# Optimization experiments

Measured on AMD Instinct MI355X. Metric: run time of the kernel, lower is better.

## Reference

```python
import jax, jax.numpy as jnp
import numpy as np

B, S0, S1 = 4, 768, 256
T = S0 + S1
W0, W1 = 2048, 1024
N, K, H = 8, 1, 256  # num_heads, num_kv_heads (MQA), head_dim
G = N // K
MAX_WAVELENGTH = 10000.0
BIG_NEG = -2.3819763e+38


def _apply_rope(x, positions):
    """RoPE: positions [B,L] applied to x [B,L,heads,H]."""
    half = x.shape[-1] // 2
    freq_exponents = (2.0 / x.shape[-1]) * jnp.arange(half, dtype=jnp.float32)
    timescale = MAX_WAVELENGTH ** freq_exponents  # [half]
    radians = positions[..., None].astype(jnp.float32) / timescale  # [B,L,half]
    radians = radians[..., None, :]  # [B,L,1,half]
    sin, cos = jnp.sin(radians), jnp.cos(radians)
    x1, x2 = jnp.split(x.astype(jnp.float32), 2, axis=-1)
    res = jnp.concatenate([x1 * cos - x2 * sin, x2 * cos + x1 * sin], axis=-1)
    return res.astype(x.dtype)


def setup_inputs() -> dict:
    key = jax.random.key(0)
    ks = jax.random.split(key, 8)
    x0 = jax.random.normal(ks[0], (B, S0, W0), dtype=jnp.float32)
    x1 = jax.random.normal(ks[1], (B, S1, W1), dtype=jnp.float32)
    positions = jnp.broadcast_to(jnp.arange(T, dtype=jnp.int32)[None, :], (B, T))
    # causal mask [B,1,T,T]
    attn_mask = jnp.broadcast_to(jnp.tril(jnp.ones((T, T), dtype=bool))[None, None], (B, 1, T, T))
    # lecun_normal on the width (in) axis
    q0_w = jax.random.normal(ks[2], (N, W0, H), dtype=jnp.float32) / np.sqrt(W0)
    kv0_w = jax.random.normal(ks[3], (2, K, W0, H), dtype=jnp.float32) / np.sqrt(W0)
    out0_w = jax.random.normal(ks[4], (N, H, W0), dtype=jnp.float32) / np.sqrt(N * H)
    q1_w = jax.random.normal(ks[5], (N, W1, H), dtype=jnp.float32) / np.sqrt(W1)
    kv1_w = jax.random.normal(ks[6], (2, K, W1, H), dtype=jnp.float32) / np.sqrt(W1)
    out1_w = jax.random.normal(ks[7], (N, H, W1), dtype=jnp.float32) / np.sqrt(N * H)
    return {"x0": x0, "x1": x1, "positions": positions, "attn_mask": attn_mask,
            "q0_w": q0_w, "kv0_w": kv0_w, "out0_w": out0_w,
            "q1_w": q1_w, "kv1_w": kv1_w, "out1_w": out1_w}


def reference(x0, x1, positions, attn_mask, q0_w, kv0_w, out0_w, q1_w, kv1_w, out1_w):
    dtype = x0.dtype
    # per-modality QKV projections (num_kv_heads != num_heads branch)
    q0 = jnp.einsum('BTD,NDH->BTNH', x0, q0_w.astype(dtype))
    k0, v0 = jnp.einsum('BSD,2KDH->2BSKH', x0, kv0_w.astype(dtype))
    q1 = jnp.einsum('BTD,NDH->BTNH', x1, q1_w.astype(dtype))
    k1, v1 = jnp.einsum('BSD,2KDH->2BSKH', x1, kv1_w.astype(dtype))
    q = jnp.concatenate([q0, q1], axis=1)  # [B,T,N,H]
    k = jnp.concatenate([k0, k1], axis=1)  # [B,T,K,H]
    v = jnp.concatenate([v0, v1], axis=1)
    q = _apply_rope(q, positions) * (H ** -0.5)
    k = _apply_rope(k, positions)
    # prefill cache init: cache_size == attn_mask.shape[-1] == T, so no padding
    idx = jnp.full((B,), T, dtype=jnp.int32)
    # GQA attention
    qg = q.reshape(B, T, K, G, H)  # 'B T (K G) H -> B T K G H'
    logits = jnp.einsum('BTKGH,BSKH->BKGTS', qg, k, preferred_element_type=jnp.float32)
    masked = jnp.where(attn_mask[:, :, None, :, :], logits, BIG_NEG)
    probs = jax.nn.softmax(masked, axis=-1).astype(dtype)
    enc = jnp.einsum('BKGTS,BSKH->BTKGH', probs, v).reshape(B, T, N, H)
    out0 = jnp.einsum('BTNH,NHD->BTD', enc[:, :S0], out0_w.astype(dtype))
    out1 = jnp.einsum('BTNH,NHD->BTD', enc[:, S0:], out1_w.astype(dtype))
    return (out0, out1, idx, k, v)
```

## Files before the change

kernel.cpp:

```cpp
#include <hip/hip_runtime.h>

typedef unsigned short u16;
typedef __attribute__((ext_vector_type(8))) short short8;
typedef __attribute__((ext_vector_type(4))) float f32x4;
typedef __attribute__((ext_vector_type(4))) unsigned short u16x4;

__device__ __forceinline__ u16 f2bf(float f){
  unsigned u = __float_as_uint(f);
  u += 0x7FFFu + ((u >> 16) & 1u);
  return (u16)(u >> 16);
}
__device__ __forceinline__ float bf2f(u16 h){
  return __uint_as_float(((unsigned)h) << 16);
}
__device__ __forceinline__ void gload16(const void* g, void* l){
  __builtin_amdgcn_global_load_lds((const __attribute__((address_space(1))) void*)g,
                                   (__attribute__((address_space(3))) void*)l, 16, 0, 0);
}
__device__ __forceinline__ f32x4 mfma16(short8 a, short8 b, f32x4 c){
  return __builtin_amdgcn_mfma_f32_16x16x32_bf16(a, b, c, 0, 0, 0);
}
__device__ __forceinline__ short8 ld8(const u16* p){
  return *reinterpret_cast<const short8*>(p);
}
__device__ __forceinline__ unsigned cvtpk(float lo, float hi){
  unsigned r;
  asm volatile("v_cvt_pk_bf16_f32 %0, %1, %2" : "=v"(r) : "v"(lo), "v"(hi));
  return r;
}

__global__ void cvt_all(const float* __restrict__ x0, const float* __restrict__ x1,
                        u16* __restrict__ x0b, u16* __restrict__ x1b){
  int bid = blockIdx.x;
  const float* s; u16* d; int i;
  if (bid < 6144){ s = x0; d = x0b; i = bid * 256 + threadIdx.x; }
  else           { s = x1; d = x1b; i = (bid - 6144) * 256 + threadIdx.x; }
  float4 v = reinterpret_cast<const float4*>(s)[i];
  u16x4 o = { f2bf(v.x), f2bf(v.y), f2bf(v.z), f2bf(v.w) };
  reinterpret_cast<u16x4*>(d)[i] = o;
}

__device__ __forceinline__
void transp_body(const float* __restrict__ S, u16* __restrict__ D,
                 int K, int C, int kb, int cb){
  __shared__ float t[32][33];
  int tx = threadIdx.x & 31, ty = threadIdx.x >> 5;
  #pragma unroll
  for (int i = ty; i < 32; i += 8)
    t[i][tx] = S[(size_t)(kb + i) * C + cb + tx];
  __syncthreads();
  #pragma unroll
  for (int i = ty; i < 32; i += 8)
    D[(size_t)(cb + i) * K + kb + tx] = f2bf(t[tx][i]);
}
__global__ __launch_bounds__(256)
void transpose_all(const float* q0_w, const float* kv0_w, const float* q1_w,
                   const float* kv1_w, const float* o0_w, const float* o1_w,
                   u16* qkv0T, u16* qkv1T, u16* o0T, u16* o1T){
  int bid = blockIdx.x;
  const float* S; u16* D; int K, C, nkc, lid;
  if (bid < 4096){
    S = q0_w; D = qkv0T; K = 2048; C = 256; lid = bid;
  } else if (bid < 5120){
    S = kv0_w; D = qkv0T + (size_t)2048*2048; K = 2048; C = 256; lid = bid - 4096;
  } else if (bid < 7168){
    S = q1_w; D = qkv1T; K = 1024; C = 256; lid = bid - 5120;
  } else if (bid < 7680){
    S = kv1_w; D = qkv1T + (size_t)2048*1024; K = 1024; C = 256; lid = bid - 7168;
  } else if (bid < 11776){
    S = o0_w; D = o0T; K = 2048; C = 2048; lid = bid - 7680;
  } else {
    S = o1_w; D = o1T; K = 2048; C = 1024; lid = bid - 11776;
  }
  nkc = (K >> 5) * (C >> 5);
  int z   = lid / nkc;
  int rem = lid - z * nkc;
  int kb  = (rem / (C >> 5)) << 5;
  int cb  = (rem % (C >> 5)) << 5;
  transp_body(S + (size_t)z * K * C, D + (size_t)z * K * C, K, C, kb, cb);
}

__device__ __forceinline__
void gemm_body(const u16* __restrict__ A, int lda, int aS, int aT, int aOff,
               const u16* __restrict__ BT, int ldbt,
               u16* __restrict__ Cb, float* __restrict__ Cf, int ldc,
               int cS, int cT, int cOff, int N, int Kd, int bid, char* smem){
  int ntx = N >> 7;
  int bm = bid / ntx;
  int bn = bid - bm * ntx;
  int row0 = bm << 7, col0 = bn << 7;
  size_t arow0 = (size_t)(row0 / aS) * aT + (row0 % aS) + aOff;
  size_t crow0 = (size_t)(row0 / cS) * cT + (row0 % cS) + cOff;
  const u16* Abase = A + arow0 * (size_t)lda;
  const u16* Bbase = BT + (size_t)col0 * ldbt;
  int tid = threadIdx.x;
  int w = tid >> 6, l = tid & 63;
  int wr = (w >> 1) << 6, wc = (w & 1) << 6;
  int lr = l & 15, g4 = l >> 4, lq = (l >> 4) << 2;
  int keyr = lr & 7;
  f32x4 acc[4][4];
  #pragma unroll
  for (int m = 0; m < 4; m++)
    #pragma unroll
    for (int n = 0; n < 4; n++)
      acc[m][n] = (f32x4){0.f, 0.f, 0.f, 0.f};
  int scol = (((tid & 7) ^ ((tid >> 3) & 7)) << 3);
  const u16* gA = Abase + (size_t)(tid >> 3) * lda + scol;
  const u16* gB = Bbase + (size_t)(tid >> 3) * ldbt + scol;
  int dsto = tid * 16;

  auto STAGE = [&](char* dst, int k0){
    gload16(gA + k0,                      dst + dsto);
    gload16(gA + (size_t)32*lda  + k0,    dst + 4096  + dsto);
    gload16(gA + (size_t)64*lda  + k0,    dst + 8192  + dsto);
    gload16(gA + (size_t)96*lda  + k0,    dst + 12288 + dsto);
    gload16(gB + k0,                      dst + 16384 + dsto);
    gload16(gB + (size_t)32*ldbt + k0,    dst + 20480 + dsto);
    gload16(gB + (size_t)64*ldbt + k0,    dst + 24576 + dsto);
    gload16(gB + (size_t)96*ldbt + k0,    dst + 28672 + dsto);
  };

  STAGE(smem, 0);
  int cur = 0;
  for (int k0 = 0; k0 < Kd; k0 += 64, cur ^= 1){
    asm volatile("" ::: "memory");
    __builtin_amdgcn_s_barrier();
    asm volatile("" ::: "memory");
    if (k0 + 64 < Kd){
      STAGE(smem + (cur ^ 1) * 32768, k0 + 64);
      asm volatile("s_waitcnt vmcnt(8)" ::: "memory");
    } else {
      asm volatile("s_waitcnt vmcnt(0)" ::: "memory");
    }
    __builtin_amdgcn_s_barrier();
    asm volatile("" ::: "memory");
    const u16* As = (const u16*)(smem + cur * 32768);
    const u16* Bs = As + 8192;
    #pragma unroll
    for (int kk = 0; kk < 2; kk++){
      int so = ((g4 + kk*4) ^ keyr) << 3;
      short8 af[4], bfr[4];
      #pragma unroll
      for (int m = 0; m < 4; m++)
        af[m] = ld8(&As[(wr + m*16 + lr)*64 + so]);
      #pragma unroll
      for (int n = 0; n < 4; n++)
        bfr[n] = ld8(&Bs[(wc + n*16 + lr)*64 + so]);
      #pragma unroll
      for (int m = 0; m < 4; m++)
        #pragma unroll
        for (int n = 0; n < 4; n++)
          acc[m][n] = mfma16(af[m], bfr[n], acc[m][n]);
    }
  }
  #pragma unroll
  for (int m = 0; m < 4; m++){
    #pragma unroll
    for (int i = 0; i < 4; i++){
      size_t r = crow0 + wr + m*16 + lq + i;
      if (Cb){
        #pragma unroll
        for (int n = 0; n < 4; n++)
          Cb[r*ldc + col0 + wc + n*16 + lr] = f2bf(acc[m][n][i]);
      } else {
        #pragma unroll
        for (int n = 0; n < 4; n++)
          Cf[r*ldc + col0 + wc + n*16 + lr] = acc[m][n][i];
      }
    }
  }
}

__global__ __launch_bounds__(256)
void gemm_qkv(const u16* __restrict__ x0b, const u16* __restrict__ qkv0T,
              const u16* __restrict__ x1b, const u16* __restrict__ qkv1T,
              u16* __restrict__ qkvb){
  extern __shared__ __align__(16) char smem[];
  int bid = blockIdx.x;
  if (bid < 480)
    gemm_body(x0b, 2048, 3072, 3072, 0, qkv0T, 2048,
              qkvb, nullptr, 2560, 768, 1024, 0, 2560, 2048, bid, smem);
  else
    gemm_body(x1b, 1024, 1024, 1024, 0, qkv1T, 1024,
              qkvb, nullptr, 2560, 256, 1024, 768, 2560, 1024, bid - 480, smem);
}

__global__ __launch_bounds__(256)
void gemm_out(const u16* __restrict__ encb, const u16* __restrict__ o0T,
              const u16* __restrict__ o1T, float* __restrict__ out0,
              float* __restrict__ out1){
  extern __shared__ __align__(16) char smem[];
  int bid = blockIdx.x;
  if (bid < 384)
    gemm_body(encb, 2048, 768, 1024, 0, o0T, 2048,
              nullptr, out0, 2048, 3072, 3072, 0, 2048, 2048, bid, smem);
  else
    gemm_body(encb, 2048, 256, 1024, 768, o1T, 2048,
              nullptr, out1, 1024, 1024, 1024, 0, 1024, 2048, bid - 384, smem);
}

__global__ void rope_kernel(u16* __restrict__ qkv, const int* __restrict__ positions,
                            float* __restrict__ k_out, float* __restrict__ v_out,
                            float* __restrict__ idx_out){
  int bt = blockIdx.x;
  int j = threadIdx.x;
  float pos = (float)positions[bt];
  float ts = powf(10000.0f, (float)j * 0.0078125f);
  float rad = pos / ts;
  float sn, cs;
  sincosf(rad, &sn, &cs);
  u16* q = qkv + (size_t)bt * 2560;
  #pragma unroll
  for (int n = 0; n < 8; n++){
    float x1 = bf2f(q[n*256 + j]);
    float x2 = bf2f(q[n*256 + 128 + j]);
    q[n*256 + j]       = f2bf((x1*cs - x2*sn) * 0.0625f);
    q[n*256 + 128 + j] = f2bf((x2*cs + x1*sn) * 0.0625f);
  }
  u16* kv = q + 2048;
  float x1 = bf2f(kv[j]), x2 = bf2f(kv[128 + j]);
  float k1 = x1*cs - x2*sn, k2 = x2*cs + x1*sn;
  kv[j] = f2bf(k1); kv[128 + j] = f2bf(k2);
  size_t ko = (size_t)bt * 256;
  k_out[ko + j] = k1;  k_out[ko + 128 + j] = k2;
  v_out[ko + j] = bf2f(kv[256 + j]);
  v_out[ko + 128 + j] = bf2f(kv[384 + j]);
  if (bt == 0 && j < 4) idx_out[j] = 1024.0f;
}

__global__ void transpose_v(const u16* __restrict__ qkv, u16* __restrict__ vT){
  __shared__ u16 t[32][33];
  int b = blockIdx.z;
  int tb = blockIdx.x * 32, hb = blockIdx.y * 32;
  int tx = threadIdx.x, ty = threadIdx.y;
  #pragma unroll
  for (int i = ty; i < 32; i += 8)
    t[i][tx] = qkv[(size_t)(b*1024 + tb + i)*2560 + 2304 + hb + tx];
  __syncthreads();
  #pragma unroll
  for (int i = ty; i < 32; i += 8)
    vT[(size_t)(b*256 + hb + i)*1024 + tb + tx] = t[tx][i];
}

__global__ __launch_bounds__(256, 2)
void attn_kernel(const u16* __restrict__ qkv, const u16* __restrict__ vT,
                 u16* __restrict__ enc){
  extern __shared__ __align__(16) char smem[];
  int bid = blockIdx.x;
  int b   = bid & 3;
  int h2  = (bid >> 2) & 1;
  int qt  = 63 - (bid >> 3);
  int tid = threadIdx.x;
  int w = tid >> 6;
  int head = h2*4 + w;
  int l = tid & 63;
  int lr = l & 15;
  int g = l >> 4;
  int lkqe  = g << 3;
  int lkq16 = g << 4;
  int q0 = qt << 4, nkv = q0 + 16;
  int swk = (lr & 7) << 4;
  int swv = ((lr >> 1) & 3) << 4;

  const char* kbase = (const char*)qkv + (size_t)b*5242880 + 4096;
  const char* vbase = (const char*)vT + (size_t)b*524288;
  const char* ksrc[4]; const char* vsrc[4];
  int kldo[4], vldo[4];
  #pragma unroll
  for (int r = 0; r < 4; r++){
    int o = r*4096 + tid*16;
    int krow = o >> 9;
    int kcol = (o & 511) ^ ((krow & 7) << 4);
    ksrc[r] = kbase + (size_t)krow*5120 + kcol;
    kldo[r] = o;
    int vrow = o >> 6;
    int vcol = (o & 63) ^ (((vrow >> 1) & 3) << 4);
    vsrc[r] = vbase + (size_t)vrow*2048 + vcol;
    vldo[r] = 16384 + o;
  }

  const u16* qb = qkv + ((size_t)(b*1024 + q0)) * 2560 + head*256;
  short8 qf[8];
  #pragma unroll
  for (int hf = 0; hf < 8; hf++)
    qf[hf] = ld8(qb + (size_t)lr*2560 + hf*32 + lkqe);

  f32x4 o_[16];
  #pragma unroll
  for (int hf = 0; hf < 16; hf++)
    o_[hf] = (f32x4){0.f,0.f,0.f,0.f};
  float mrow = -3.0e38f, lrow = 0.f;

  auto STAGE = [&](int buf, int kt){
    char* dst = smem + buf*32768;
    #pragma unroll
    for (int r = 0; r < 4; r++)
      gload16(ksrc[r] + (size_t)kt*5120, dst + kldo[r]);
    #pragma unroll
    for (int r = 0; r < 4; r++)
      gload16(vsrc[r] + (size_t)kt*2, dst + vldo[r]);
  };

  STAGE(0, 0);
  int cur = 0;
  for (int kt = 0; kt < nkv; kt += 32, cur ^= 1){
    asm volatile("" ::: "memory");
    __builtin_amdgcn_s_barrier();
    asm volatile("" ::: "memory");
    if (kt + 32 < nkv){
      STAGE(cur ^ 1, kt + 32);
      asm volatile("s_waitcnt vmcnt(8)" ::: "memory");
    } else {
      asm volatile("s_waitcnt vmcnt(0)" ::: "memory");
    }
    __builtin_amdgcn_s_barrier();
    asm volatile("" ::: "memory");

    const char* Kb = smem + cur*32768;
    const char* Vb = Kb + 16384;
    f32x4 s[2];
    s[0] = (f32x4){0.f,0.f,0.f,0.f};
    s[1] = (f32x4){0.f,0.f,0.f,0.f};
    __builtin_amdgcn_s_setprio(1);
    #pragma unroll
    for (int hf = 0; hf < 8; hf++){
      int colb = (hf*64 + lkq16) ^ swk;
      short8 k0 = *(const short8*)(Kb + (size_t)(lr     )*512 + colb);
      short8 k1 = *(const short8*)(Kb + (size_t)(lr + 16)*512 + colb);
      s[0] = mfma16(k0, qf[hf], s[0]);
      s[1] = mfma16(k1, qf[hf], s[1]);
    }
    __builtin_amdgcn_s_setprio(0);
    if (kt + 32 > q0){
      #pragma unroll
      for (int cf = 0; cf < 2; cf++)
        #pragma unroll
        for (int i = 0; i < 4; i++){
          int kv_g = kt + cf*16 + g*4 + i;
          if (kv_g > q0 + lr) s[cf][i] = -1.0e30f;
        }
    }
    float m8 = fmaxf(fmaxf(fmaxf(s[0][0], s[0][1]), fmaxf(s[0][2], s[0][3])),
                     fmaxf(fmaxf(s[1][0], s[1][1]), fmaxf(s[1][2], s[1][3])));
    m8 = fmaxf(m8, __shfl_xor(m8, 16, 64));
    m8 = fmaxf(m8, __shfl_xor(m8, 32, 64));
    bool nd = (m8 > mrow + 8.f);
    if (__ballot(nd)){
      float mn = fmaxf(mrow, m8);
      float corr = __expf(mrow - mn);
      mrow = mn;
      lrow *= corr;
      #pragma unroll
      for (int hf = 0; hf < 16; hf++)
        #pragma unroll
        for (int i = 0; i < 4; i++)
          o_[hf][i] *= corr;
    }
    float p[2][4];
    #pragma unroll
    for (int cf = 0; cf < 2; cf++)
      #pragma unroll
      for (int i = 0; i < 4; i++)
        p[cf][i] = __expf(s[cf][i] - mrow);
    float sum8 = p[0][0] + p[0][1] + p[0][2] + p[0][3]
               + p[1][0] + p[1][1] + p[1][2] + p[1][3];
    sum8 += __shfl_xor(sum8, 16, 64);
    sum8 += __shfl_xor(sum8, 32, 64);
    lrow += sum8;
    unsigned A0 = cvtpk(p[0][0], p[0][1]);
    unsigned A1 = cvtpk(p[0][2], p[0][3]);
    unsigned B0 = cvtpk(p[1][0], p[1][1]);
    unsigned B1 = cvtpk(p[1][2], p[1][3]);
    unsigned sp0 = (unsigned)__shfl_xor((int)(g < 2 ? A0 : B0), 16, 64);
    unsigned sp1 = (unsigned)__shfl_xor((int)(g < 2 ? A1 : B1), 16, 64);
    unsigned c0  = (unsigned)__shfl_xor((int)(l < 32 ? B0 : A0), 32, 64);
    unsigned c1  = (unsigned)__shfl_xor((int)(l < 32 ? B1 : A1), 32, 64);
    unsigned pc0 = (unsigned)__shfl_xor((int)c0, 16, 64);
    unsigned pc1 = (unsigned)__shfl_xor((int)c1, 16, 64);
    union { unsigned u[4]; short8 v; } pf;
    pf.u[0] = (g == 0) ? A0 : (g == 1) ? pc0 : (g == 2) ? c0  : sp0;
    pf.u[1] = (g == 0) ? A1 : (g == 1) ? pc1 : (g == 2) ? c1  : sp1;
    pf.u[2] = (g == 0) ? sp0 : (g == 1) ? c0 : (g == 2) ? pc0 : B0;
    pf.u[3] = (g == 0) ? sp1 : (g == 1) ? c1 : (g == 2) ? pc1 : B1;
    __builtin_amdgcn_s_setprio(1);
    #pragma unroll
    for (int hf = 0; hf < 16; hf++){
      const char* vr = Vb + (size_t)(hf*16 + lr)*64;
      short8 v0 = *(const short8*)(vr + (lkq16 ^ swv));
      o_[hf] = mfma16(v0, pf.v, o_[hf]);
    }
    __builtin_amdgcn_s_setprio(0);
  }
  u16* eb = enc + ((size_t)(b*1024 + q0 + lr)) * 2048 + head*256;
  float inv = 1.0f / lrow;
  #pragma unroll
  for (int hf = 0; hf < 16; hf++){
    u16x4 st = { f2bf(o_[hf][0] * inv), f2bf(o_[hf][1] * inv),
                 f2bf(o_[hf][2] * inv), f2bf(o_[hf][3] * inv) };
    *reinterpret_cast<u16x4*>(eb + hf*16 + g*4) = st;
  }
}

extern "C" void kernel_launch(void* const* d_in, const int* in_sizes, int n_in,
                              void* d_out, int out_size, void* d_ws, size_t ws_size,
                              hipStream_t stream){
  const float* x0     = (const float*)d_in[0];
  const float* x1     = (const float*)d_in[1];
  const int*   pos    = (const int*)d_in[2];
  const float* q0_w   = (const float*)d_in[4];
  const float* kv0_w  = (const float*)d_in[5];
  const float* out0_w = (const float*)d_in[6];
  const float* q1_w   = (const float*)d_in[7];
  const float* kv1_w  = (const float*)d_in[8];
  const float* out1_w = (const float*)d_in[9];

  float* out  = (float*)d_out;
  float* out0 = out;
  float* out1 = out + 6291456;
  float* idxp = out + 7340032;
  float* kout = out + 7340036;
  float* vout = out + 8388612;

  char* ws = (char*)d_ws;
  size_t off = 0;
  auto alloc = [&](size_t bytes){
    void* p = ws + off;
    off = (off + bytes + 255) & ~(size_t)255;
    return p;
  };
  u16* x0b   = (u16*)alloc((size_t)6291456 * 2);
  u16* x1b   = (u16*)alloc((size_t)1048576 * 2);
  u16* qkv0T = (u16*)alloc((size_t)2560 * 2048 * 2);
  u16* qkv1T = (u16*)alloc((size_t)2560 * 1024 * 2);
  u16* o0T   = (u16*)alloc((size_t)2048 * 2048 * 2);
  u16* o1T   = (u16*)alloc((size_t)1024 * 2048 * 2);
  u16* qkvb  = (u16*)alloc((size_t)4096 * 2560 * 2);
  u16* vTb   = (u16*)alloc((size_t)4 * 256 * 1024 * 2);
  u16* encb  = (u16*)alloc((size_t)4096 * 2048 * 2);

  hipFuncSetAttribute((const void*)attn_kernel,
                      hipFuncAttributeMaxDynamicSharedMemorySize, 65536);
  hipFuncSetAttribute((const void*)gemm_qkv,
                      hipFuncAttributeMaxDynamicSharedMemorySize, 65536);
  hipFuncSetAttribute((const void*)gemm_out,
                      hipFuncAttributeMaxDynamicSharedMemorySize, 65536);

  cvt_all<<<7168, 256, 0, stream>>>(x0, x1, x0b, x1b);
  transpose_all<<<13824, 256, 0, stream>>>(q0_w, kv0_w, q1_w, kv1_w, out0_w, out1_w,
                                           qkv0T, qkv1T, o0T, o1T);

  gemm_qkv<<<640, 256, 65536, stream>>>(x0b, qkv0T, x1b, qkv1T, qkvb);

  rope_kernel<<<4096, 128, 0, stream>>>(qkvb, pos, kout, vout, idxp);
  transpose_v<<<dim3(32, 8, 4), dim3(32,8), 0, stream>>>(qkvb, vTb);
  attn_kernel<<<512, 256, 65536, stream>>>(qkvb, vTb, encb);

  gemm_out<<<448, 256, 65536, stream>>>(encb, o0T, o1T, out0, out1);
}
```

Before: 168.0 us.

## Process two 16-row query tiles per wave in attention to reuse K/V loads

Each attention wave now handles 32 query rows as two 16-row halves that share every K and V fragment read from LDS, with separate softmax state per half. The block count halves to 256 and launch bounds drop to one block per SM to make room for the doubled accumulators. The goal is to halve K/V staging and LDS traffic per query row. The cost is fewer blocks (256 across the GPU's compute units), lower occupancy, more register pressure and coarser causal load balance.

```diff
diff --git a/kernel.cpp b/kernel.cpp
--- a/kernel.cpp
+++ b/kernel.cpp
@@ -242,14 +242,14 @@
     vT[(size_t)(b*256 + hb + i)*1024 + tb + tx] = t[tx][i];
 }
 
-__global__ __launch_bounds__(256, 2)
+__global__ __launch_bounds__(256, 1)
 void attn_kernel(const u16* __restrict__ qkv, const u16* __restrict__ vT,
                  u16* __restrict__ enc){
   extern __shared__ __align__(16) char smem[];
   int bid = blockIdx.x;
   int b   = bid & 3;
   int h2  = (bid >> 2) & 1;
-  int qt  = 63 - (bid >> 3);
+  int qt  = 31 - (bid >> 3);
   int tid = threadIdx.x;
   int w = tid >> 6;
   int head = h2*4 + w;
@@ -258,7 +258,7 @@
   int g = l >> 4;
   int lkqe  = g << 3;
   int lkq16 = g << 4;
-  int q0 = qt << 4, nkv = q0 + 16;
+  int q0 = qt << 5, nkv = q0 + 32;
   int swk = (lr & 7) << 4;
   int swv = ((lr >> 1) & 3) << 4;
 
@@ -280,16 +280,21 @@
   }
 
   const u16* qb = qkv + ((size_t)(b*1024 + q0)) * 2560 + head*256;
-  short8 qf[8];
-  #pragma unroll
-  for (int hf = 0; hf < 8; hf++)
-    qf[hf] = ld8(qb + (size_t)lr*2560 + hf*32 + lkqe);
-
-  f32x4 o_[16];
-  #pragma unroll
-  for (int hf = 0; hf < 16; hf++)
-    o_[hf] = (f32x4){0.f,0.f,0.f,0.f};
-  float mrow = -3.0e38f, lrow = 0.f;
+  short8 qf[2][8];
+  #pragma unroll
+  for (int qh = 0; qh < 2; qh++)
+    #pragma unroll
+    for (int hf = 0; hf < 8; hf++)
+      qf[qh][hf] = ld8(qb + (size_t)(qh*16 + lr)*2560 + hf*32 + lkqe);
+
+  f32x4 o_[2][16];
+  #pragma unroll
+  for (int qh = 0; qh < 2; qh++)
+    #pragma unroll
+    for (int hf = 0; hf < 16; hf++)
+      o_[qh][hf] = (f32x4){0.f,0.f,0.f,0.f};
+  float mrow[2] = { -3.0e38f, -3.0e38f };
+  float lrow[2] = { 0.f, 0.f };
 
   auto STAGE = [&](int buf, int kt){
     char* dst = smem + buf*32768;
@@ -318,86 +323,113 @@
 
     const char* Kb = smem + cur*32768;
     const char* Vb = Kb + 16384;
-    f32x4 s[2];
-    s[0] = (f32x4){0.f,0.f,0.f,0.f};
-    s[1] = (f32x4){0.f,0.f,0.f,0.f};
+    f32x4 s[2][2];
+    #pragma unroll
+    for (int qh = 0; qh < 2; qh++)
+      #pragma unroll
+      for (int cf = 0; cf < 2; cf++)
+        s[qh][cf] = (f32x4){0.f,0.f,0.f,0.f};
     __builtin_amdgcn_s_setprio(1);
     #pragma unroll
     for (int hf = 0; hf < 8; hf++){
       int colb = (hf*64 + lkq16) ^ swk;
       short8 k0 = *(const short8*)(Kb + (size_t)(lr     )*512 + colb);
       short8 k1 = *(const short8*)(Kb + (size_t)(lr + 16)*512 + colb);
-      s[0] = mfma16(k0, qf[hf], s[0]);
-      s[1] = mfma16(k1, qf[hf], s[1]);
+      s[0][0] = mfma16(k0, qf[0][hf], s[0][0]);
+      s[0][1] = mfma16(k1, qf[0][hf], s[0][1]);
+      s[1][0] = mfma16(k0, qf[1][hf], s[1][0]);
+      s[1][1] = mfma16(k1, qf[1][hf], s[1][1]);
     }
     __builtin_amdgcn_s_setprio(0);
     if (kt + 32 > q0){
       #pragma unroll
+      for (int qh = 0; qh < 2; qh++)
+        #pragma unroll
+        for (int cf = 0; cf < 2; cf++)
+          #pragma unroll
+          for (int i = 0; i < 4; i++){
+            int kv_g = kt + cf*16 + g*4 + i;
+            if (kv_g > q0 + qh*16 + lr) s[qh][cf][i] = -1.0e30f;
+          }
+    }
+    float m8[2];
+    #pragma unroll
+    for (int qh = 0; qh < 2; qh++){
+      float m = fmaxf(fmaxf(fmaxf(s[qh][0][0], s[qh][0][1]), fmaxf(s[qh][0][2], s[qh][0][3])),
+                      fmaxf(fmaxf(s[qh][1][0], s[qh][1][1]), fmaxf(s[qh][1][2], s[qh][1][3])));
+      m = fmaxf(m, __shfl_xor(m, 16, 64));
+      m = fmaxf(m, __shfl_xor(m, 32, 64));
+      m8[qh] = m;
+    }
+    bool nd = (m8[0] > mrow[0] + 8.f) || (m8[1] > mrow[1] + 8.f);
+    if (__ballot(nd)){
+      #pragma unroll
+      for (int qh = 0; qh < 2; qh++){
+        float mn = fmaxf(mrow[qh], m8[qh]);
+        float corr = __expf(mrow[qh] - mn);
+        mrow[qh] = mn;
+        lrow[qh] *= corr;
+        #pragma unroll
+        for (int hf = 0; hf < 16; hf++)
+          #pragma unroll
+          for (int i = 0; i < 4; i++)
+            o_[qh][hf][i] *= corr;
+      }
+    }
+    float p[2][2][4];
+    #pragma unroll
+    for (int qh = 0; qh < 2; qh++){
+      #pragma unroll
       for (int cf = 0; cf < 2; cf++)
         #pragma unroll
-        for (int i = 0; i < 4; i++){
-          int kv_g = kt + cf*16 + g*4 + i;
-          if (kv_g > q0 + lr) s[cf][i] = -1.0e30f;
-        }
-    }
-    float m8 = fmaxf(fmaxf(fmaxf(s[0][0], s[0][1]), fmaxf(s[0][2], s[0][3])),
-                     fmaxf(fmaxf(s[1][0], s[1][1]), fmaxf(s[1][2], s[1][3])));
-    m8 = fmaxf(m8, __shfl_xor(m8, 16, 64));
-    m8 = fmaxf(m8, __shfl_xor(m8, 32, 64));
-    bool nd = (m8 > mrow + 8.f);
-    if (__ballot(nd)){
-      float mn = fmaxf(mrow, m8);
-      float corr = __expf(mrow - mn);
-      mrow = mn;
-      lrow *= corr;
-      #pragma unroll
-      for (int hf = 0; hf < 16; hf++)
-        #pragma unroll
         for (int i = 0; i < 4; i++)
-          o_[hf][i] *= corr;
-    }
-    float p[2][4];
-    #pragma unroll
-    for (int cf = 0; cf < 2; cf++)
-      #pragma unroll
-      for (int i = 0; i < 4; i++)
-        p[cf][i] = __expf(s[cf][i] - mrow);
-    float sum8 = p[0][0] + p[0][1] + p[0][2] + p[0][3]
-               + p[1][0] + p[1][1] + p[1][2] + p[1][3];
-    sum8 += __shfl_xor(sum8, 16, 64);
-    sum8 += __shfl_xor(sum8, 32, 64);
-    lrow += sum8;
-    unsigned A0 = cvtpk(p[0][0], p[0][1]);
-    unsigned A1 = cvtpk(p[0][2], p[0][3]);
-    unsigned B0 = cvtpk(p[1][0], p[1][1]);
-    unsigned B1 = cvtpk(p[1][2], p[1][3]);
-    unsigned sp0 = (unsigned)__shfl_xor((int)(g < 2 ? A0 : B0), 16, 64);
-    unsigned sp1 = (unsigned)__shfl_xor((int)(g < 2 ? A1 : B1), 16, 64);
-    unsigned c0  = (unsigned)__shfl_xor((int)(l < 32 ? B0 : A0), 32, 64);
-    unsigned c1  = (unsigned)__shfl_xor((int)(l < 32 ? B1 : A1), 32, 64);
-    unsigned pc0 = (unsigned)__shfl_xor((int)c0, 16, 64);
-    unsigned pc1 = (unsigned)__shfl_xor((int)c1, 16, 64);
-    union { unsigned u[4]; short8 v; } pf;
-    pf.u[0] = (g == 0) ? A0 : (g == 1) ? pc0 : (g == 2) ? c0  : sp0;
-    pf.u[1] = (g == 0) ? A1 : (g == 1) ? pc1 : (g == 2) ? c1  : sp1;
-    pf.u[2] = (g == 0) ? sp0 : (g == 1) ? c0 : (g == 2) ? pc0 : B0;
-    pf.u[3] = (g == 0) ? sp1 : (g == 1) ? c1 : (g == 2) ? pc1 : B1;
+          p[qh][cf][i] = __expf(s[qh][cf][i] - mrow[qh]);
+      float sum8 = p[qh][0][0] + p[qh][0][1] + p[qh][0][2] + p[qh][0][3]
+                 + p[qh][1][0] + p[qh][1][1] + p[qh][1][2] + p[qh][1][3];
+      sum8 += __shfl_xor(sum8, 16, 64);
+      sum8 += __shfl_xor(sum8, 32, 64);
+      lrow[qh] += sum8;
+    }
+    short8 pfv[2];
+    #pragma unroll
+    for (int qh = 0; qh < 2; qh++){
+      unsigned A0 = cvtpk(p[qh][0][0], p[qh][0][1]);
+      unsigned A1 = cvtpk(p[qh][0][2], p[qh][0][3]);
+      unsigned B0 = cvtpk(p[qh][1][0], p[qh][1][1]);
+      unsigned B1 = cvtpk(p[qh][1][2], p[qh][1][3]);
+      unsigned sp0 = (unsigned)__shfl_xor((int)(g < 2 ? A0 : B0), 16, 64);
+      unsigned sp1 = (unsigned)__shfl_xor((int)(g < 2 ? A1 : B1), 16, 64);
+      unsigned c0  = (unsigned)__shfl_xor((int)(l < 32 ? B0 : A0), 32, 64);
+      unsigned c1  = (unsigned)__shfl_xor((int)(l < 32 ? B1 : A1), 32, 64);
+      unsigned pc0 = (unsigned)__shfl_xor((int)c0, 16, 64);
+      unsigned pc1 = (unsigned)__shfl_xor((int)c1, 16, 64);
+      union { unsigned u[4]; short8 v; } pf;
+      pf.u[0] = (g == 0) ? A0 : (g == 1) ? pc0 : (g == 2) ? c0  : sp0;
+      pf.u[1] = (g == 0) ? A1 : (g == 1) ? pc1 : (g == 2) ? c1  : sp1;
+      pf.u[2] = (g == 0) ? sp0 : (g == 1) ? c0 : (g == 2) ? pc0 : B0;
+      pf.u[3] = (g == 0) ? sp1 : (g == 1) ? c1 : (g == 2) ? pc1 : B1;
+      pfv[qh] = pf.v;
+    }
     __builtin_amdgcn_s_setprio(1);
     #pragma unroll
     for (int hf = 0; hf < 16; hf++){
       const char* vr = Vb + (size_t)(hf*16 + lr)*64;
       short8 v0 = *(const short8*)(vr + (lkq16 ^ swv));
-      o_[hf] = mfma16(v0, pf.v, o_[hf]);
+      o_[0][hf] = mfma16(v0, pfv[0], o_[0][hf]);
+      o_[1][hf] = mfma16(v0, pfv[1], o_[1][hf]);
     }
     __builtin_amdgcn_s_setprio(0);
   }
-  u16* eb = enc + ((size_t)(b*1024 + q0 + lr)) * 2048 + head*256;
-  float inv = 1.0f / lrow;
-  #pragma unroll
-  for (int hf = 0; hf < 16; hf++){
-    u16x4 st = { f2bf(o_[hf][0] * inv), f2bf(o_[hf][1] * inv),
-                 f2bf(o_[hf][2] * inv), f2bf(o_[hf][3] * inv) };
-    *reinterpret_cast<u16x4*>(eb + hf*16 + g*4) = st;
+  #pragma unroll
+  for (int qh = 0; qh < 2; qh++){
+    u16* eb = enc + ((size_t)(b*1024 + q0 + qh*16 + lr)) * 2048 + head*256;
+    float inv = 1.0f / lrow[qh];
+    #pragma unroll
+    for (int hf = 0; hf < 16; hf++){
+      u16x4 st = { f2bf(o_[qh][hf][0] * inv), f2bf(o_[qh][hf][1] * inv),
+                   f2bf(o_[qh][hf][2] * inv), f2bf(o_[qh][hf][3] * inv) };
+      *reinterpret_cast<u16x4*>(eb + hf*16 + g*4) = st;
+    }
   }
 }
 
@@ -453,7 +485,7 @@
 
   rope_kernel<<<4096, 128, 0, stream>>>(qkvb, pos, kout, vout, idxp);
   transpose_v<<<dim3(32, 8, 4), dim3(32,8), 0, stream>>>(qkvb, vTb);
-  attn_kernel<<<512, 256, 65536, stream>>>(qkvb, vTb, encb);
+  attn_kernel<<<256, 256, 65536, stream>>>(qkvb, vTb, encb);
 
   gemm_out<<<448, 256, 65536, stream>>>(encb, o0T, o1T, out0, out1);
 }
```

Result: slower. 194.0 us (+15.5%).
